# Kernel optimization log

Hardware: AMD Instinct MI355X
Metric: run time of the kernel (lower is better)

Reference implementation:

```python
import jax, jax.numpy as jnp
import numpy as np

B, NQ, NC, DC, DY = 4, 4096, 4096, 2, 8


def setup_inputs() -> dict:
    key = jax.random.key(0)
    k1, k2, k3 = jax.random.split(key, 3)
    x_query = jax.random.normal(k1, (B, NQ, DC), dtype=jnp.float32)
    x_context = jax.random.normal(k2, (B, NC, DC), dtype=jnp.float32)
    y_context = jax.random.normal(k3, (B, NC, DY), dtype=jnp.float32)
    log_length_scale = jnp.asarray(np.log(0.1), dtype=jnp.float32)
    return {
        "x_query": x_query,
        "x_context": x_context,
        "y_context": y_context,
        "log_length_scale": log_length_scale,
    }


def reference(x_query, x_context, y_context, log_length_scale):
    # Squared Euclidean distances: (B, NQ, NC).
    # cdist followed by .pow(2) == squared distance, so compute d2 directly.
    diff = x_query[:, :, None, :] - x_context[:, None, :, :]  # (B,NQ,NC,DC)
    d2 = jnp.sum(diff * diff, axis=-1)                         # (B,NQ,NC)
    length_scale = jnp.exp(log_length_scale)
    weights = jnp.exp(-d2 / (2.0 * length_scale ** 2))         # RBF kernel
    density = jnp.sum(weights, axis=-1, keepdims=True)         # (B,NQ,1)
    weights_norm = weights / (density + 1e-8)
    y_query = jnp.einsum('bqc,bcd->bqd', weights_norm, y_context)  # (B,NQ,DY)
    return jnp.concatenate([y_query, density], axis=-1)        # (B,NQ,DY+1)
```

## Files before the change

kernel.cpp:

```cpp
#include <hip/hip_runtime.h>


#define BB 4
#define NQ 4096
#define NC 4096
#define DY 8
#define NBQ (BB * NQ)

#if __has_builtin(__builtin_amdgcn_exp2f)
#define EXP2F(x) __builtin_amdgcn_exp2f(x)
#else
#define EXP2F(x) exp2f(x)
#endif

typedef short bf16x8 __attribute__((ext_vector_type(8)));
typedef float f32x4  __attribute__((ext_vector_type(4)));
typedef float f32x2  __attribute__((ext_vector_type(2)));

__device__ __forceinline__ short f2bf(float v) {
    return (short)(__builtin_bit_cast(unsigned, v) >> 16);
}
__device__ __forceinline__ unsigned fbits(float v) {
    return __builtin_bit_cast(unsigned, v);
}
__device__ __forceinline__ unsigned bfpair(float w0, float w1) {
#if __has_builtin(__builtin_amdgcn_perm)
    return __builtin_amdgcn_perm(fbits(w1), fbits(w0), 0x07060302u);
#else
    return (fbits(w1) & 0xFFFF0000u) | (fbits(w0) >> 16);
#endif
}

#define GSPLIT 8
#define CCHUNK (NC / GSPLIT)
#define NPAIR (CCHUNK / 2)
#define KSTEPS (CCHUNK / 32)
#define QPB 128
#define NT 8
#define KPW (KSTEPS / 4)
#define QB (NBQ / QPB)
#define JS ((size_t)GSPLIT * NBQ)
#define WS_FLOATS ((size_t)(DY + 1) * GSPLIT * NBQ)

__global__ __launch_bounds__(256, 4) void setconv_accum_mfma(
    const float* __restrict__ xq, const float* __restrict__ xc,
    const float* __restrict__ yc, const float* __restrict__ lls,
    float* __restrict__ ws)
{
    __shared__ float4 sxp[NPAIR];
    __shared__ float2 shp[NPAIR];
    __shared__ __attribute__((aligned(16)))
        unsigned short yfrag[CCHUNK / 8][16][8];

    const int bid  = blockIdx.x;
    const int gs   = bid & (GSPLIT - 1);
    const int qb   = bid >> 3;
    const int b    = qb >> 5;
    const int tid  = threadIdx.x;
    const int lane = tid & 63;
    const int wv   = tid >> 6;
    const int m    = lane & 15;
    const int quad = lane >> 4;

    const float L    = lls[0];
    const float negk = -0.72134752044448f * EXP2F(L * -2.8853900817779268f);

    {
        const float4* xcp = (const float4*)(((const float2*)xc) + (size_t)b * NC + gs * CCHUNK);
        const float4 v = xcp[tid];
        sxp[tid] = make_float4(v.x, v.z, v.y, v.w);
        shp[tid] = make_float2(negk * fmaf(v.x, v.x, v.y * v.y),
                               negk * fmaf(v.z, v.z, v.w * v.w));
    }
    {
        const float4* yp = (const float4*)(yc + ((size_t)b * NC + gs * CCHUNK) * DY);
#pragma unroll
        for (int i = 0; i < 2; ++i) {
            const int c = tid + 256 * i;
            const float4 A  = yp[2 * c + 0];
            const float4 Bv = yp[2 * c + 1];
            const int g = c >> 3, j = c & 7;
            unsigned short* dst = &yfrag[g][0][j];
            dst[0 * 8] = (unsigned short)f2bf(A.x);
            dst[1 * 8] = (unsigned short)f2bf(A.y);
            dst[2 * 8] = (unsigned short)f2bf(A.z);
            dst[3 * 8] = (unsigned short)f2bf(A.w);
            dst[4 * 8] = (unsigned short)f2bf(Bv.x);
            dst[5 * 8] = (unsigned short)f2bf(Bv.y);
            dst[6 * 8] = (unsigned short)f2bf(Bv.z);
            dst[7 * 8] = (unsigned short)f2bf(Bv.w);
        }
        unsigned* yf32 = (unsigned*)yfrag;
#pragma unroll
        for (int i = 0; i < 8; ++i) {
            const int v = tid + 256 * i;
            const int g = v >> 5, r = v & 31;
            yf32[g * 64 + 32 + r] = (r < 4) ? 0x3F803F80u : 0u;
        }
    }

    float A0s[NT], A1s[NT], A2s[NT];
#pragma unroll
    for (int t = 0; t < NT; ++t) {
        const int q = qb * QPB + t * 16 + m;
        const float2 qv = ((const float2*)xq)[q];
        A0s[t] = negk * fmaf(qv.x, qv.x, qv.y * qv.y);
        A1s[t] = -2.f * negk * qv.x;
        A2s[t] = -2.f * negk * qv.y;
    }

    f32x4 acc[NT];
#pragma unroll
    for (int t = 0; t < NT; ++t) acc[t] = (f32x4){0.f, 0.f, 0.f, 0.f};

    __syncthreads();

    for (int ks = 0; ks < KPW; ++ks) {
        const int s = wv * KPW + ks;
        const bf16x8 bfrag = *(const bf16x8*)&yfrag[s * 4 + quad][m][0];
        float4 xp[4]; float2 hp[4];
#pragma unroll
        for (int jp = 0; jp < 4; ++jp) {
            const int P = s * 16 + quad * 4 + jp;
            xp[jp] = sxp[P];
            hp[jp] = shp[P];
        }
#pragma unroll
        for (int t = 0; t < NT; ++t) {
            const f32x2 a0 = {A0s[t], A0s[t]};
            const f32x2 a1 = {A1s[t], A1s[t]};
            const f32x2 a2 = {A2s[t], A2s[t]};
            unsigned au[4];
#pragma unroll
            for (int jp = 0; jp < 4; ++jp) {
                const f32x2 cx2 = {xp[jp].x, xp[jp].y};
                const f32x2 cy2 = {xp[jp].z, xp[jp].w};
                const f32x2 hc2 = {hp[jp].x, hp[jp].y};
                f32x2 tt = __builtin_elementwise_fma(cx2, a1, hc2 + a0);
                tt = __builtin_elementwise_fma(cy2, a2, tt);
                au[jp] = bfpair(EXP2F(tt.x), EXP2F(tt.y));
            }
            const bf16x8 af = __builtin_bit_cast(bf16x8, *(uint4*)au);
            acc[t] = __builtin_amdgcn_mfma_f32_16x16x32_bf16(af, bfrag, acc[t], 0, 0, 0);
        }
    }

    __syncthreads();
    float4* rb = (float4*)&yfrag[0][0][0];
    for (int h = 0; h < 4; ++h) {
#pragma unroll
        for (int u = 0; u < 2; ++u) {
            const int t = h * 2 + u;
            rb[(u * 4 + wv) * 64 + lane] =
                make_float4(acc[t][0], acc[t][1], acc[t][2], acc[t][3]);
        }
        __syncthreads();
        if (wv == h && m <= 8) {
#pragma unroll
            for (int u = 0; u < 2; ++u) {
                const int t = h * 2 + u;
                float4 v = rb[(u * 4 + 0) * 64 + lane];
#pragma unroll
                for (int w = 1; w < 4; ++w) {
                    const float4 z = rb[(u * 4 + w) * 64 + lane];
                    v.x += z.x; v.y += z.y; v.z += z.z; v.w += z.w;
                }
                *(float4*)&ws[(size_t)m * JS + (size_t)gs * NBQ +
                              (size_t)qb * QPB + t * 16 + quad * 4] = v;
            }
        }
        __syncthreads();
    }
}

__global__ __launch_bounds__(256) void setconv_reduce(
    const float* __restrict__ ws, float* __restrict__ out)
{
    __shared__ float part[4][64][DY + 1];
    const int tid  = threadIdx.x;
    const int qi   = tid & 63;
    const int sg   = tid >> 6;
    const int base = blockIdx.x * 64;
    const int bq   = base + qi;

#pragma unroll
    for (int j = 0; j < DY + 1; ++j) {
        float s = 0.f;
#pragma unroll
        for (int k = 0; k < GSPLIT / 4; ++k) {
            const int split = sg * (GSPLIT / 4) + k;
            s += ws[(size_t)j * JS + (size_t)split * NBQ + bq];
        }
        part[sg][qi][j] = s;
    }
    __syncthreads();

    for (int it = tid; it < 64 * (DY + 1); it += 256) {
        const int q2 = it / (DY + 1);
        const int j  = it - q2 * (DY + 1);
        const float den = part[0][q2][DY] + part[1][q2][DY] +
                          part[2][q2][DY] + part[3][q2][DY];
        float v;
        if (j == DY) {
            v = den;
        } else {
            const float s = part[0][q2][j] + part[1][q2][j] +
                            part[2][q2][j] + part[3][q2][j];
            v = s / (den + 1e-8f);
        }
        out[(size_t)base * (DY + 1) + it] = v;
    }
}

#define FSPLIT 8
#define FCCH (NC / FSPLIT)

__global__ __launch_bounds__(256) void setconv_zero(float4* __restrict__ out) {
    out[blockIdx.x * 256 + threadIdx.x] = make_float4(0.f, 0.f, 0.f, 0.f);
}

__global__ __launch_bounds__(256) void setconv_accum_atomic(
    const float* __restrict__ xq, const float* __restrict__ xc,
    const float* __restrict__ yc, const float* __restrict__ lls,
    float* __restrict__ out)
{
    const int bid   = blockIdx.x;
    const int split = bid & (FSPLIT - 1);
    const int qblk  = (bid / FSPLIT) & (NQ / 256 - 1);
    const int b     = bid / (FSPLIT * (NQ / 256));
    const int q     = qblk * 256 + threadIdx.x;

    const float L    = lls[0];
    const float negk = -0.72134752044448f * EXP2F(L * -2.8853900817779268f);

    const float2 qv = ((const float2*)xq)[b * NQ + q];
    const float qx0 = qv.x, qy0 = qv.y;

    float acc[DY], den = 0.f;
#pragma unroll
    for (int j = 0; j < DY; ++j) acc[j] = 0.f;

    const float2* __restrict__ xcp = ((const float2*)xc) + (size_t)b * NC;
    const float4* __restrict__ ycp = ((const float4*)yc) + (size_t)b * NC * 2;

    const int c0 = split * FCCH;
#pragma unroll 4
    for (int c = c0; c < c0 + FCCH; ++c) {
        const float2 cv = xcp[c];
        const float4 y0 = ycp[2 * c + 0];
        const float4 y1 = ycp[2 * c + 1];
        const float dx = qx0 - cv.x;
        const float dy = qy0 - cv.y;
        const float d2 = fmaf(dy, dy, dx * dx);
        const float w  = EXP2F(d2 * negk);
        den += w;
        acc[0] = fmaf(w, y0.x, acc[0]);
        acc[1] = fmaf(w, y0.y, acc[1]);
        acc[2] = fmaf(w, y0.z, acc[2]);
        acc[3] = fmaf(w, y0.w, acc[3]);
        acc[4] = fmaf(w, y1.x, acc[4]);
        acc[5] = fmaf(w, y1.y, acc[5]);
        acc[6] = fmaf(w, y1.z, acc[6]);
        acc[7] = fmaf(w, y1.w, acc[7]);
    }

    float* o = out + (size_t)(b * NQ + q) * (DY + 1);
#pragma unroll
    for (int j = 0; j < DY; ++j) atomicAdd(o + j, acc[j]);
    atomicAdd(o + DY, den);
}

__global__ __launch_bounds__(256) void setconv_norm(float* __restrict__ out) {
    const int q = blockIdx.x * 256 + threadIdx.x;
    float* o = out + (size_t)q * (DY + 1);
    const float inv = 1.0f / (o[DY] + 1e-8f);
#pragma unroll
    for (int j = 0; j < DY; ++j) o[j] *= inv;
}

extern "C" void kernel_launch(void* const* d_in, const int* in_sizes, int n_in,
                              void* d_out, int out_size, void* d_ws, size_t ws_size,
                              hipStream_t stream) {
    const float* xq  = (const float*)d_in[0];
    const float* xc  = (const float*)d_in[1];
    const float* yc  = (const float*)d_in[2];
    const float* lls = (const float*)d_in[3];
    float* out = (float*)d_out;

    if (ws_size >= WS_FLOATS * sizeof(float)) {
        float* ws = (float*)d_ws;
        setconv_accum_mfma<<<QB * GSPLIT, 256, 0, stream>>>(xq, xc, yc, lls, ws);
        setconv_reduce<<<NBQ / 64, 256, 0, stream>>>(ws, out);
    } else {
        setconv_zero<<<(NBQ * (DY + 1)) / 1024, 256, 0, stream>>>((float4*)out);
        setconv_accum_atomic<<<BB * (NQ / 256) * FSPLIT, 256, 0, stream>>>(xq, xc, yc, lls, out);
        setconv_norm<<<NBQ / 256, 256, 0, stream>>>(out);
    }
}
```

Measured before the change: 73.85 us.

## Fuse accumulation and reduction into one cooperative kernel with grid sync

Merges the MFMA accumulation kernel and the cross-split reduction kernel into a single cooperative launch that uses a grid-wide barrier between phases. After the barrier each block reduces 16 queries across the GSPLIT partial sums and writes normalized outputs. This removes a second kernel launch and its launch gap. In exchange it adds grid-sync cost, requires all blocks (QB*GSPLIT = 1024) to be co-resident, and keeps the old two-kernel path as a fallback if the cooperative launch fails.

```diff
diff --git a/kernel.cpp b/kernel.cpp
--- a/kernel.cpp
+++ b/kernel.cpp
@@ -1,4 +1,7 @@
 #include <hip/hip_runtime.h>
+#include <hip/hip_cooperative_groups.h>
+
+namespace cg = cooperative_groups;
 
 
 #define BB 4
@@ -39,19 +42,16 @@
 #define NT 8
 #define KPW (KSTEPS / 4)
 #define QB (NBQ / QPB)
+#define NBLK (QB * GSPLIT)
 #define JS ((size_t)GSPLIT * NBQ)
 #define WS_FLOATS ((size_t)(DY + 1) * GSPLIT * NBQ)
 
-__global__ __launch_bounds__(256, 4) void setconv_accum_mfma(
+__device__ __forceinline__ void accum_phase(
     const float* __restrict__ xq, const float* __restrict__ xc,
     const float* __restrict__ yc, const float* __restrict__ lls,
-    float* __restrict__ ws)
-{
-    __shared__ float4 sxp[NPAIR];
-    __shared__ float2 shp[NPAIR];
-    __shared__ __attribute__((aligned(16)))
-        unsigned short yfrag[CCHUNK / 8][16][8];
-
+    float* __restrict__ ws,
+    float4* sxp, float2* shp, unsigned short (*yfrag)[16][8])
+{
     const int bid  = blockIdx.x;
     const int gs   = bid & (GSPLIT - 1);
     const int qb   = bid >> 3;
@@ -171,6 +171,50 @@
         }
         __syncthreads();
     }
+}
+
+__global__ __launch_bounds__(256, 4) void setconv_fused(
+    const float* __restrict__ xq, const float* __restrict__ xc,
+    const float* __restrict__ yc, const float* __restrict__ lls,
+    float* __restrict__ ws, float* __restrict__ out)
+{
+    __shared__ float4 sxp[NPAIR];
+    __shared__ float2 shp[NPAIR];
+    __shared__ __attribute__((aligned(16)))
+        unsigned short yfrag[CCHUNK / 8][16][8];
+
+    accum_phase(xq, xc, yc, lls, ws, sxp, shp, yfrag);
+
+    __threadfence();
+    cg::this_grid().sync();
+
+    const int tid = threadIdx.x;
+    if (tid < 16 * (DY + 1)) {
+        const int q2 = tid / (DY + 1);
+        const int j  = tid - q2 * (DY + 1);
+        const int bq = blockIdx.x * 16 + q2;
+        float s = 0.f, den = 0.f;
+#pragma unroll
+        for (int k = 0; k < GSPLIT; ++k) {
+            s   += __hip_atomic_load(&ws[(size_t)j  * JS + (size_t)k * NBQ + bq],
+                                     __ATOMIC_RELAXED, __HIP_MEMORY_SCOPE_AGENT);
+            den += __hip_atomic_load(&ws[(size_t)DY * JS + (size_t)k * NBQ + bq],
+                                     __ATOMIC_RELAXED, __HIP_MEMORY_SCOPE_AGENT);
+        }
+        out[(size_t)bq * (DY + 1) + j] = (j == DY) ? den : s / (den + 1e-8f);
+    }
+}
+
+__global__ __launch_bounds__(256, 4) void setconv_accum_mfma(
+    const float* __restrict__ xq, const float* __restrict__ xc,
+    const float* __restrict__ yc, const float* __restrict__ lls,
+    float* __restrict__ ws)
+{
+    __shared__ float4 sxp[NPAIR];
+    __shared__ float2 shp[NPAIR];
+    __shared__ __attribute__((aligned(16)))
+        unsigned short yfrag[CCHUNK / 8][16][8];
+    accum_phase(xq, xc, yc, lls, ws, sxp, shp, yfrag);
 }
 
 __global__ __launch_bounds__(256) void setconv_reduce(
@@ -289,8 +333,15 @@
 
     if (ws_size >= WS_FLOATS * sizeof(float)) {
         float* ws = (float*)d_ws;
-        setconv_accum_mfma<<<QB * GSPLIT, 256, 0, stream>>>(xq, xc, yc, lls, ws);
-        setconv_reduce<<<NBQ / 64, 256, 0, stream>>>(ws, out);
+        void* args[] = {(void*)&xq, (void*)&xc, (void*)&yc,
+                        (void*)&lls, (void*)&ws, (void*)&out};
+        hipError_t e = hipLaunchCooperativeKernel(
+            (const void*)setconv_fused, dim3(NBLK), dim3(256), args, 0, stream);
+        if (e != hipSuccess) {
+            (void)hipGetLastError();
+            setconv_accum_mfma<<<NBLK, 256, 0, stream>>>(xq, xc, yc, lls, ws);
+            setconv_reduce<<<NBQ / 64, 256, 0, stream>>>(ws, out);
+        }
     } else {
         setconv_zero<<<(NBQ * (DY + 1)) / 1024, 256, 0, stream>>>((float4*)out);
         setconv_accum_atomic<<<BB * (NQ / 256) * FSPLIT, 256, 0, stream>>>(xq, xc, yc, lls, out);
```

New measurement: 208.4 us. 182% more time.
